# Kernel optimization log

Hardware: AMD Instinct MI355X
Metric: run time of the kernel (lower is better)

## Reference

```python
import jax, jax.numpy as jnp
import numpy as np

SP = 4          # window/split size
HEADS = 8       # num_heads
SHIFTS = (0, 2) # shift_sizes


def _rel_pos_index(sp):
    # Same construction as the torch buffer `relative_position_index`.
    coords = np.stack(np.meshgrid(np.arange(sp), np.arange(sp), indexing='ij'))  # [2,sp,sp]
    coords = coords.reshape(2, -1)                                               # [2, sp*sp]
    rel = coords[:, :, None] - coords[:, None, :]                                # [2, N, N]
    rel = rel.transpose(1, 2, 0).astype(np.int64)                                # [N, N, 2]
    rel[..., 0] += sp - 1
    rel[..., 1] += sp - 1
    rel[..., 0] *= 2 * sp - 1
    return rel.sum(-1)  # [N, N]


def _window_attend(xh, qkv_w, lepe_w, bias, sp, heads, scale):
    # xh: [B, c, H, W] with c = split_dim
    B, c, H, W = xh.shape
    hd = c // heads
    h, w = H // sp, W // sp
    # 1x1 conv to qkv (no bias)
    qkv = jnp.einsum('oi,bihw->bohw', qkv_w, xh)
    q, k, v = jnp.split(qkv, 3, axis=1)
    # depthwise 3x3 LePE on v
    lepe = jax.lax.conv_general_dilated(v, lepe_w, (1, 1), 'SAME',
                                        feature_group_count=c)

    def part(t):
        # 'b (c head) (h hsp) (w wsp) -> (b h w) head (hsp wsp) c'
        t = t.reshape(B, hd, heads, h, sp, w, sp)
        t = t.transpose(0, 3, 5, 2, 4, 6, 1)  # b,h,w,head,hsp,wsp,hd
        return t.reshape(B * h * w, heads, sp * sp, hd)

    q, k, v, lepe = map(part, (q, k, v, lepe))
    attn = jnp.einsum('nhqc,nhkc->nhqk', q * scale, k) + bias[None]  # [N,heads,16,16]
    attn = jax.nn.softmax(attn, axis=-1)
    out = jnp.einsum('nhqk,nhkc->nhqc', attn, v) + lepe
    # inverse rearrange back to [B, c, H, W]
    out = out.reshape(B, h, w, heads, sp, sp, hd)
    out = out.transpose(0, 6, 3, 1, 4, 2, 5).reshape(B, c, H, W)
    return out


def setup_inputs() -> dict:
    key = jax.random.key(0)
    k1, k2, k3, k4 = jax.random.split(key, 4)
    x = jax.random.normal(k1, (8, 128, 192, 192), dtype=jnp.float32)
    qkv_w = jax.random.normal(k2, (192, 64), dtype=jnp.float32) * 0.05   # [3*split_dim, split_dim]
    lepe_w = jax.random.normal(k3, (64, 1, 3, 3), dtype=jnp.float32) * 0.05  # depthwise
    bias_table = jax.random.normal(k4, (49, 8), dtype=jnp.float32) * 0.02    # [(2sp-1)^2, heads]
    return {'x': x, 'qkv_w': qkv_w, 'lepe_w': lepe_w, 'bias_table': bias_table}


def reference(x, qkv_w, lepe_w, bias_table):
    B, C, H, W = x.shape
    c = C // 2
    hd = c // HEADS
    scale = hd ** -0.5
    idx = _rel_pos_index(SP)  # static numpy [16,16]
    bias = bias_table[idx.reshape(-1)].reshape(SP * SP, SP * SP, HEADS)
    bias = bias.transpose(2, 0, 1)  # [heads, 16, 16]

    results = []
    for s in SHIFTS:
        # NOTE: faithful to source, roll is over dims (1,2) = (channel, height)
        xs = jnp.roll(x, (-s, -s), axis=(1, 2)) if s > 0 else x
        halves = (xs[:, :c], xs[:, c:])
        outs = [_window_attend(xh, qkv_w, lepe_w, bias, SP, HEADS, scale)
                for xh in halves]
        if s > 0:
            outs = [jnp.roll(o, (s, s), axis=(1, 2)) for o in outs]
        results.append(jnp.concatenate(outs, axis=1))
    return results[0] + results[1]
```

## Files before the change

### kernel.cpp

```cpp
#include <hip/hip_runtime.h>

typedef __attribute__((ext_vector_type(8))) short short8v;
typedef __attribute__((ext_vector_type(8))) __fp16 h8v;
typedef __attribute__((ext_vector_type(2))) __fp16 h2v;
typedef __attribute__((ext_vector_type(4))) float f32x4;

#define XSTRIDE 136

__device__ inline unsigned short f2bf(float f) {
    unsigned u = __builtin_bit_cast(unsigned, f);
    return (unsigned short)((u + 0x7FFFu + ((u >> 16) & 1u)) >> 16);
}

__device__ inline float dot2(h2v a, h2v b, float c) {
#if __has_builtin(__builtin_amdgcn_fdot2)
    return __builtin_amdgcn_fdot2(a, b, c, false);
#else
    return c + (float)a[0] * (float)b[0] + (float)a[1] * (float)b[1];
#endif
}
__device__ inline h2v pk2h(float a, float b) {
#if __has_builtin(__builtin_amdgcn_cvt_pkrtz)
    return __builtin_bit_cast(h2v, __builtin_amdgcn_cvt_pkrtz(a, b));
#else
    h2v r; r[0] = (__fp16)a; r[1] = (__fp16)b; return r;
#endif
}
__device__ inline float fexp2(float x) {
#if __has_builtin(__builtin_amdgcn_exp2f)
    return __builtin_amdgcn_exp2f(x);
#else
    return __expf(x * 0.6931471805599453f);
#endif
}

__global__ __launch_bounds__(256) void prep_weights(const float* __restrict__ qkv_w,
                                                    __fp16* __restrict__ wf) {
    int it = blockIdx.x * 256 + threadIdx.x;
    if (it >= 1536) return;
    int l = it & 63, frag = it >> 6;
    int which = frag >> 3, nt = (frag >> 1) & 3, kst = frag & 1;
    const float* src = qkv_w + (which * 64 + nt * 16 + (l & 15)) * 64 + kst * 32 + (l >> 4) * 8;
    h8v pk;
    #pragma unroll
    for (int j = 0; j < 8; ++j) pk[j] = (__fp16)src[j];
    *reinterpret_cast<h8v*>(wf + it * 8) = pk;
}

__global__ __launch_bounds__(256) void prep_x(const float* __restrict__ x,
                                              __fp16* __restrict__ xh) {
    const int xt = blockIdx.x;
    const int y  = blockIdx.y;
    const int b  = blockIdx.z;
    const int x0 = xt * 32;
    __shared__ float buf[128 * 33];

    for (int it = threadIdx.x; it < 1024; it += 256) {
        int c = it >> 3, xq = it & 7;
        const float4 v = *reinterpret_cast<const float4*>(
            x + ((b * 128 + c) * 192 + y) * 192 + x0 + xq * 4);
        float* d = &buf[c * 33 + xq * 4];
        d[0] = v.x; d[1] = v.y; d[2] = v.z; d[3] = v.w;
    }
    __syncthreads();

    for (int it = threadIdx.x; it < 512; it += 256) {
        int xl = it >> 4, c8 = it & 15;
        h8v pk;
        #pragma unroll
        for (int j = 0; j < 8; ++j) pk[j] = (__fp16)buf[(c8 * 8 + j) * 33 + xl];
        __fp16* dst = xh + (((size_t)(b * 192 + y) * 192) + x0 + xl) * XSTRIDE + c8 * 8;
        __builtin_memcpy(dst, &pk, 16);
    }
    if (threadIdx.x < 32) {
        int xl = threadIdx.x;
        h2v d2; d2[0] = (__fp16)buf[0 * 33 + xl]; d2[1] = (__fp16)buf[1 * 33 + xl];
        __fp16* dst = xh + (((size_t)(b * 192 + y) * 192) + x0 + xl) * XSTRIDE + 128;
        __builtin_memcpy(dst, &d2, 4);
    }
}

template<int SHIFT, bool ACCUM>
__global__ __launch_bounds__(256) void swin_main(
    const __fp16* __restrict__ xh,
    const __fp16* __restrict__ wfrag,
    const float* __restrict__ lepe_w,
    const float* __restrict__ bias_table,
    float* __restrict__ out)
{
    const int bx = blockIdx.x;
    const int wy = bx / 12, strip = bx % 12;
    const int half = blockIdx.y, b = blockIdx.z;
    const int tid = threadIdx.x;
    const int w = tid >> 6, l = tid & 63;

    __shared__ __fp16 pool[9216];
    __shared__ __fp16 qs[64 * 64];
    __shared__ __fp16 ks[64 * 64];
    __shared__ float  bias_s[392];
    __shared__ __fp16 lepe_s[576];

    for (int i = tid; i < 392; i += 256) bias_s[i] = bias_table[i] * 1.4426950408889634f;
    for (int i = tid; i < 576; i += 256) {
        int d = i & 7, rest = i >> 3;
        int j = rest % 9, h = rest / 9;
        lepe_s[i] = (__fp16)lepe_w[(d * 8 + h) * 9 + j];
    }

    const int ry0 = wy * 4 - 1, rx0 = strip * 16 - 1;
    for (int it = tid; it < 864; it += 256) {
        const int pos = it >> 3, slot = it & 7;
        const int py = pos / 18, px = pos - py * 18;
        const int ry = ry0 + py, rx = rx0 + px;
        h8v val;
        #pragma unroll
        for (int j = 0; j < 8; ++j) val[j] = (__fp16)0.f;
        if (ry >= 0 && ry < 192 && rx >= 0 && rx < 192) {
            int phys = ry + SHIFT; if (phys >= 192) phys -= 192;
            const int srcslot = slot ^ (pos & 7);
            const __fp16* src = xh + (((size_t)(b * 192 + phys) * 192) + rx) * XSTRIDE
                                   + half * 64 + srcslot * 8 + SHIFT;
            __builtin_memcpy(&val, src, 16);
        }
        *reinterpret_cast<h8v*>(&pool[pos * 64 + slot * 8]) = val;
    }
    __syncthreads();

    const int tok16 = l & 15, g = l >> 4;
    h8v Aq[2], Av[3][2];
    {
        const int posq = (1 + (tok16 >> 2)) * 18 + w * 4 + 1 + (tok16 & 3);
        #pragma unroll
        for (int kst = 0; kst < 2; ++kst) {
            int chunk = (kst * 4 + g) ^ (posq & 7);
            Aq[kst] = *reinterpret_cast<const h8v*>(&pool[posq * 64 + chunk * 8]);
        }
        #pragma unroll
        for (int mt = 0; mt < 3; ++mt) {
            int t = mt * 16 + tok16;
            int posv = (t < 36) ? ((t / 6) * 18 + w * 4 + (t % 6)) : 0;
            #pragma unroll
            for (int kst = 0; kst < 2; ++kst) {
                int chunk = (kst * 4 + g) ^ (posv & 7);
                Av[mt][kst] = *reinterpret_cast<const h8v*>(&pool[posv * 64 + chunk * 8]);
            }
        }
    }
    __syncthreads();

    #pragma unroll
    for (int nt = 0; nt < 4; ++nt) {
        h8v Bq[2], Bk[2], Bv[2];
        #pragma unroll
        for (int kst = 0; kst < 2; ++kst) {
            Bq[kst] = *reinterpret_cast<const h8v*>(wfrag + (((0 * 8 + nt * 2 + kst) * 64 + l) * 8));
            Bk[kst] = *reinterpret_cast<const h8v*>(wfrag + (((1 * 8 + nt * 2 + kst) * 64 + l) * 8));
            Bv[kst] = *reinterpret_cast<const h8v*>(wfrag + (((2 * 8 + nt * 2 + kst) * 64 + l) * 8));
        }
        f32x4 aQ = {0.f,0.f,0.f,0.f}, aK = {0.f,0.f,0.f,0.f};
        f32x4 aV[3];
        #pragma unroll
        for (int mt = 0; mt < 3; ++mt) aV[mt] = (f32x4){0.f,0.f,0.f,0.f};
        #pragma unroll
        for (int kst = 0; kst < 2; ++kst) {
            aQ = __builtin_amdgcn_mfma_f32_16x16x32_f16(Aq[kst], Bq[kst], aQ, 0, 0, 0);
            aK = __builtin_amdgcn_mfma_f32_16x16x32_f16(Aq[kst], Bk[kst], aK, 0, 0, 0);
            #pragma unroll
            for (int mt = 0; mt < 3; ++mt)
                aV[mt] = __builtin_amdgcn_mfma_f32_16x16x32_f16(Av[mt][kst], Bv[kst], aV[mt], 0, 0, 0);
        }
        const int ch  = nt * 16 + tok16;
        const int chp = (ch & 7) * 8 + (ch >> 3);
        #pragma unroll
        for (int r = 0; r < 4; ++r) {
            const int qtok = w * 16 + 4 * g + r;
            const int pb = (((chp >> 3) ^ (qtok & 7)) * 8 + (chp & 7));
            qs[qtok * 64 + pb] = (__fp16)(aQ[r] * 0.5101293f);
            ks[qtok * 64 + pb] = (__fp16)aK[r];
        }
        #pragma unroll
        for (int mt = 0; mt < 3; ++mt)
            #pragma unroll
            for (int r = 0; r < 4; ++r) {
                const int t = mt * 16 + 4 * g + r;
                if (t < 36) {
                    const int pb = (((chp >> 3) ^ (t & 7)) * 8 + (chp & 7));
                    pool[(w * 36 + t) * 64 + pb] = (__fp16)aV[mt][r];
                }
            }
    }
    __syncthreads();

    {
        const int h = l >> 3, tqp = l & 7;
        const int qy0 = tqp >> 2, qx0 = tqp & 3;
        const __fp16* vv = &pool[w * 36 * 64];

        const int ox = strip * 16 + w * 4 + qx0;
        int oy0 = wy * 4 + qy0 + SHIFT;     if (oy0 >= 192) oy0 -= 192;
        int oy1 = wy * 4 + qy0 + 2 + SHIFT; if (oy1 >= 192) oy1 -= 192;
        const int ddelta = (oy1 - oy0) * 192;
        int idx0[8];
        float prev0[8], prev1[8];
        #pragma unroll
        for (int d = 0; d < 8; ++d) {
            const int oc = half * 64 + ((d * 8 + h + SHIFT) & 63);
            idx0[d] = ((b * 128 + oc) * 192 + oy0) * 192 + ox;
            if (ACCUM) { prev0[d] = out[idx0[d]]; prev1[d] = out[idx0[d] + ddelta]; }
        }

        const int t0 = w * 16 + tqp, t1 = t0 + 8;
        h8v q0 = *reinterpret_cast<const h8v*>(&qs[t0 * 64 + (h ^ (t0 & 7)) * 8]);
        h8v q1 = *reinterpret_cast<const h8v*>(&qs[t1 * 64 + (h ^ (t1 & 7)) * 8]);
        const h2v* q0p = reinterpret_cast<const h2v*>(&q0);
        const h2v* q1p = reinterpret_cast<const h2v*>(&q1);

        h2v scp0[8], scp1[8];
        float den0 = 0.f, den1 = 0.f;
        #pragma unroll
        for (int tkp = 0; tkp < 8; ++tkp) {
            float e0[2], e1[2];
            #pragma unroll
            for (int u = 0; u < 2; ++u) {
                const int tk = tkp * 2 + u;
                const int kt = w * 16 + tk;
                h8v kr = *reinterpret_cast<const h8v*>(&ks[kt * 64 + (h ^ (kt & 7)) * 8]);
                const h2v* kp = reinterpret_cast<const h2v*>(&kr);
                float s0 = 0.f, s1 = 0.f;
                #pragma unroll
                for (int i = 0; i < 4; ++i) { s0 = dot2(q0p[i], kp[i], s0); s1 = dot2(q1p[i], kp[i], s1); }
                const int ky = tk >> 2, kx = tk & 3;
                s0 += bias_s[((qy0 - ky + 3) * 7 + (qx0 - kx + 3)) * 8 + h];
                s1 += bias_s[((qy0 + 2 - ky + 3) * 7 + (qx0 - kx + 3)) * 8 + h];
                e0[u] = fexp2(s0); e1[u] = fexp2(s1);
            }
            den0 += e0[0] + e0[1]; den1 += e1[0] + e1[1];
            scp0[tkp] = pk2h(e0[0], e0[1]);
            scp1[tkp] = pk2h(e1[0], e1[1]);
        }
        const float inv0 = 1.f / den0, inv1 = 1.f / den1;
        const h2v ip0 = pk2h(inv0, inv0), ip1 = pk2h(inv1, inv1);

        h2v o0pk[4], o1pk[4];
        #pragma unroll
        for (int j = 0; j < 4; ++j) { o0pk[j] = pk2h(0.f, 0.f); o1pk[j] = pk2h(0.f, 0.f); }
        #pragma unroll
        for (int tkp = 0; tkp < 8; ++tkp) {
            const h2v w0 = scp0[tkp] * ip0;
            const h2v w1 = scp1[tkp] * ip1;
            #pragma unroll
            for (int u = 0; u < 2; ++u) {
                const int tk = tkp * 2 + u;
                const int t = (1 + (tk >> 2)) * 6 + 1 + (tk & 3);
                h8v vr = *reinterpret_cast<const h8v*>(&vv[t * 64 + (h ^ (t & 7)) * 8]);
                const h2v* vp = reinterpret_cast<const h2v*>(&vr);
                h2v b0; b0[0] = w0[u]; b0[1] = w0[u];
                h2v b1; b1[0] = w1[u]; b1[1] = w1[u];
                #pragma unroll
                for (int j = 0; j < 4; ++j) {
                    o0pk[j] += b0 * vp[j];
                    o1pk[j] += b1 * vp[j];
                }
            }
        }

        #pragma unroll
        for (int dy = 0; dy < 3; ++dy)
            #pragma unroll
            for (int dx = 0; dx < 3; ++dx) {
                const int ta = (qy0 + dy) * 6 + qx0 + dx;
                const int tb = ta + 12;
                h8v v0 = *reinterpret_cast<const h8v*>(&vv[ta * 64 + (h ^ (ta & 7)) * 8]);
                h8v v1 = *reinterpret_cast<const h8v*>(&vv[tb * 64 + (h ^ (tb & 7)) * 8]);
                h8v lw = *reinterpret_cast<const h8v*>(&lepe_s[(h * 9 + dy * 3 + dx) * 8]);
                const h2v* v0p = reinterpret_cast<const h2v*>(&v0);
                const h2v* v1p = reinterpret_cast<const h2v*>(&v1);
                const h2v* lwp = reinterpret_cast<const h2v*>(&lw);
                #pragma unroll
                for (int j = 0; j < 4; ++j) {
                    o0pk[j] += v0p[j] * lwp[j];
                    o1pk[j] += v1p[j] * lwp[j];
                }
            }

        #pragma unroll
        for (int d = 0; d < 8; ++d) {
            const float a0 = (float)o0pk[d >> 1][d & 1];
            const float a1 = (float)o1pk[d >> 1][d & 1];
            if (ACCUM) { out[idx0[d]] = prev0[d] + a0; out[idx0[d] + ddelta] = prev1[d] + a1; }
            else       { out[idx0[d]] = a0;            out[idx0[d] + ddelta] = a1; }
        }
    }
}

template<int SHIFT, bool ACCUM>
__global__ __launch_bounds__(256) void swin_fb(
    const float* __restrict__ x, const float* __restrict__ qkv_w,
    const float* __restrict__ lepe_w, const float* __restrict__ bias_table,
    float* __restrict__ out)
{
    const int C = 128, HH = 192, WW = 192;
    const int win = blockIdx.x, wy = win / 48, wx = win % 48;
    const int half = blockIdx.y, b = blockIdx.z, tid = threadIdx.x;
    __shared__ short xpA[8 * 64 * 8];
    __shared__ float vs[64 * 37], qsf[64 * 17], ksf[64 * 17];
    __shared__ float bias_s[392], lepe_s[576];
    const int ys0 = wy * 4, xs0 = wx * 4;
    for (int i = tid; i < 392; i += 256) bias_s[i] = bias_table[i];
    for (int i = tid; i < 576; i += 256) lepe_s[i] = lepe_w[i];
    for (int item = tid; item < 512; item += 256) {
        const int slot = item >> 6, l = item & 63, kst = slot & 1;
        int p = 0; bool tvalid = true;
        if (slot < 6) { int t48 = (slot >> 1) * 16 + (l & 15); tvalid = (t48 < 36); p = t48; }
        else { int ti = l & 15; p = (1 + (ti >> 2)) * 6 + 1 + (ti & 3); }
        const int c0 = kst * 32 + (l >> 4) * 8;
        short8v pk;
        #pragma unroll
        for (int j = 0; j < 8; ++j) pk[j] = 0;
        if (tvalid) {
            int py = p / 6, px = p - py * 6;
            int ry = ys0 - 1 + py, rx = xs0 - 1 + px;
            if (ry >= 0 && ry < HH && rx >= 0 && rx < WW) {
                int oy = ry + SHIFT; if (oy >= HH) oy -= HH;
                #pragma unroll
                for (int j = 0; j < 8; ++j) {
                    int oc = half * 64 + c0 + j + SHIFT; if (oc >= C) oc -= C;
                    pk[j] = (short)f2bf(x[((b * C + oc) * HH + oy) * WW + rx]);
                }
            }
        }
        *reinterpret_cast<short8v*>(&xpA[item * 8]) = pk;
    }
    const int w = tid >> 6, l = tid & 63, nn = l & 15, g = l >> 4;
    short8v Bq[2], Bk[2], Bv[2];
    #pragma unroll
    for (int kst = 0; kst < 2; ++kst) {
        const int coff = kst * 32 + g * 8;
        const float* s0 = qkv_w + (w * 16 + nn) * 64 + coff;
        const float* s1 = qkv_w + (64 + w * 16 + nn) * 64 + coff;
        const float* s2 = qkv_w + (128 + w * 16 + nn) * 64 + coff;
        short8v p0, p1, p2;
        #pragma unroll
        for (int j = 0; j < 8; ++j) { p0[j] = (short)f2bf(s0[j]); p1[j] = (short)f2bf(s1[j]); p2[j] = (short)f2bf(s2[j]); }
        Bq[kst] = p0; Bk[kst] = p1; Bv[kst] = p2;
    }
    __syncthreads();
    {
        short8v Aq[2], Avf[3][2];
        #pragma unroll
        for (int kst = 0; kst < 2; ++kst)
            Aq[kst] = *reinterpret_cast<const short8v*>(&xpA[((6 + kst) * 64 + l) * 8]);
        #pragma unroll
        for (int mt = 0; mt < 3; ++mt)
            #pragma unroll
            for (int kst = 0; kst < 2; ++kst)
                Avf[mt][kst] = *reinterpret_cast<const short8v*>(&xpA[((mt * 2 + kst) * 64 + l) * 8]);
        f32x4 aQ = {0,0,0,0}, aK = {0,0,0,0}; f32x4 aV[3];
        #pragma unroll
        for (int mt = 0; mt < 3; ++mt) aV[mt] = (f32x4){0,0,0,0};
        #pragma unroll
        for (int kst = 0; kst < 2; ++kst) {
            aQ = __builtin_amdgcn_mfma_f32_16x16x32_bf16(Aq[kst], Bq[kst], aQ, 0, 0, 0);
            aK = __builtin_amdgcn_mfma_f32_16x16x32_bf16(Aq[kst], Bk[kst], aK, 0, 0, 0);
            #pragma unroll
            for (int mt = 0; mt < 3; ++mt)
                aV[mt] = __builtin_amdgcn_mfma_f32_16x16x32_bf16(Avf[mt][kst], Bv[kst], aV[mt], 0, 0, 0);
        }
        const int ch = w * 16 + nn;
        #pragma unroll
        for (int r = 0; r < 4; ++r) { qsf[ch * 17 + g * 4 + r] = aQ[r]; ksf[ch * 17 + g * 4 + r] = aK[r]; }
        #pragma unroll
        for (int mt = 0; mt < 3; ++mt)
            #pragma unroll
            for (int r = 0; r < 4; ++r) { int tok = mt * 16 + g * 4 + r; if (tok < 36) vs[ch * 37 + tok] = aV[mt][r]; }
    }
    __syncthreads();
    {
        const int tq = tid & 15, h = (tid >> 4) & 7, dh = tid >> 7;
        const int qy = tq >> 2, qx = tq & 3;
        const float scale = 0.35355339059327373f;
        float qreg[8];
        #pragma unroll
        for (int d = 0; d < 8; ++d) qreg[d] = qsf[(d * 8 + h) * 17 + tq] * scale;
        float sc[16]; float m = -1e30f;
        #pragma unroll
        for (int tk = 0; tk < 16; ++tk) {
            float s = 0.f;
            #pragma unroll
            for (int d = 0; d < 8; ++d) s += qreg[d] * ksf[(d * 8 + h) * 17 + tk];
            s += bias_s[((qy - (tk >> 2) + 3) * 7 + (qx - (tk & 3) + 3)) * 8 + h];
            sc[tk] = s; m = fmaxf(m, s);
        }
        float den = 0.f;
        #pragma unroll
        for (int tk = 0; tk < 16; ++tk) { sc[tk] = __expf(sc[tk] - m); den += sc[tk]; }
        const float inv = 1.f / den;
        float lw[4][9];
        #pragma unroll
        for (int dd = 0; dd < 4; ++dd) {
            int ch = (dh * 4 + dd) * 8 + h;
            #pragma unroll
            for (int j = 0; j < 9; ++j) lw[dd][j] = lepe_s[ch * 9 + j];
        }
        float o[4] = {0,0,0,0};
        #pragma unroll
        for (int tk = 0; tk < 16; ++tk) {
            int p = (1 + (tk >> 2)) * 6 + 1 + (tk & 3); float s = sc[tk];
            #pragma unroll
            for (int dd = 0; dd < 4; ++dd) o[dd] += s * vs[((dh * 4 + dd) * 8 + h) * 37 + p];
        }
        int oy = ys0 + qy + SHIFT; if (oy >= HH) oy -= HH;
        const int irx = xs0 + qx;
        #pragma unroll
        for (int dd = 0; dd < 4; ++dd) {
            const int ch = (dh * 4 + dd) * 8 + h;
            float val = o[dd] * inv;
            #pragma unroll
            for (int dy = 0; dy < 3; ++dy)
                #pragma unroll
                for (int dx = 0; dx < 3; ++dx)
                    val += vs[ch * 37 + (qy + dy) * 6 + (qx + dx)] * lw[dd][dy * 3 + dx];
            const int oc = half * 64 + ((ch + SHIFT) & 63);
            const int oidx = ((b * C + oc) * HH + oy) * WW + irx;
            if (ACCUM) out[oidx] += val; else out[oidx] = val;
        }
    }
}

extern "C" void kernel_launch(void* const* d_in, const int* in_sizes, int n_in,
                              void* d_out, int out_size, void* d_ws, size_t ws_size,
                              hipStream_t stream) {
    const float* x          = (const float*)d_in[0];
    const float* qkv_w      = (const float*)d_in[1];
    const float* lepe_w     = (const float*)d_in[2];
    const float* bias_table = (const float*)d_in[3];
    float* out = (float*)d_out;

    const size_t XH_BYTES = 8UL * 192 * 192 * XSTRIDE * 2;
    const size_t NEED = 32768 + XH_BYTES;

    if (ws_size >= NEED) {
        __fp16* wf = (__fp16*)d_ws;
        __fp16* xh = (__fp16*)((char*)d_ws + 32768);
        prep_weights<<<6, 256, 0, stream>>>(qkv_w, wf);
        prep_x<<<dim3(6, 192, 8), 256, 0, stream>>>(x, xh);
        dim3 grid(576, 2, 8);
        swin_main<0, false><<<grid, 256, 0, stream>>>(xh, wf, lepe_w, bias_table, out);
        swin_main<2, true ><<<grid, 256, 0, stream>>>(xh, wf, lepe_w, bias_table, out);
    } else {
        dim3 grid(48 * 48, 2, 8);
        swin_fb<0, false><<<grid, 256, 0, stream>>>(x, qkv_w, lepe_w, bias_table, out);
        swin_fb<2, true ><<<grid, 256, 0, stream>>>(x, qkv_w, lepe_w, bias_table, out);
    }
}
```

Measured before the change: 325.4 us.

## Pre-roll fp16 input per shift and pass Q through lane shuffles instead of LDS

prep_x now writes two fully rolled, unpadded fp16 copies of x (shift 0 and shift 2), so the main kernel loads aligned 16-byte vectors with no row wrap or channel offset. Q is no longer staged in shared memory. It is packed to half2 and redistributed with cross-lane shuffles into each lane's registers for the attention step. This removes the unaligned XSTRIDE-136 loads and the Q LDS buffer, but doubles the prep write traffic and workspace and adds shuffle and select work.

```diff
diff --git a/kernel.cpp b/kernel.cpp
--- a/kernel.cpp
+++ b/kernel.cpp
@@ -4,8 +4,6 @@
 typedef __attribute__((ext_vector_type(8))) __fp16 h8v;
 typedef __attribute__((ext_vector_type(2))) __fp16 h2v;
 typedef __attribute__((ext_vector_type(4))) float f32x4;
-
-#define XSTRIDE 136
 
 __device__ inline unsigned short f2bf(float f) {
     unsigned u = __builtin_bit_cast(unsigned, f);
@@ -32,6 +30,13 @@
 #else
     return __expf(x * 0.6931471805599453f);
 #endif
+}
+__device__ inline h2v sel_pack(int x01, int x23, int y01, int y23, int rSel) {
+    unsigned sx = (unsigned)(rSel < 2 ? x01 : x23);
+    unsigned sy = (unsigned)(rSel < 2 ? y01 : y23);
+    unsigned ex = (rSel & 1) ? (sx >> 16) : (sx & 0xffffu);
+    unsigned ey = (rSel & 1) ? (sy >> 16) : (sy & 0xffffu);
+    return __builtin_bit_cast(h2v, (unsigned)(ex | (ey << 16)));
 }
 
 __global__ __launch_bounds__(256) void prep_weights(const float* __restrict__ qkv_w,
@@ -48,7 +53,8 @@
 }
 
 __global__ __launch_bounds__(256) void prep_x(const float* __restrict__ x,
-                                              __fp16* __restrict__ xh) {
+                                              __fp16* __restrict__ xbf0,
+                                              __fp16* __restrict__ xbf2) {
     const int xt = blockIdx.x;
     const int y  = blockIdx.y;
     const int b  = blockIdx.z;
@@ -64,25 +70,27 @@
     }
     __syncthreads();
 
-    for (int it = threadIdx.x; it < 512; it += 256) {
-        int xl = it >> 4, c8 = it & 15;
-        h8v pk;
-        #pragma unroll
-        for (int j = 0; j < 8; ++j) pk[j] = (__fp16)buf[(c8 * 8 + j) * 33 + xl];
-        __fp16* dst = xh + (((size_t)(b * 192 + y) * 192) + x0 + xl) * XSTRIDE + c8 * 8;
-        __builtin_memcpy(dst, &pk, 16);
-    }
-    if (threadIdx.x < 32) {
-        int xl = threadIdx.x;
-        h2v d2; d2[0] = (__fp16)buf[0 * 33 + xl]; d2[1] = (__fp16)buf[1 * 33 + xl];
-        __fp16* dst = xh + (((size_t)(b * 192 + y) * 192) + x0 + xl) * XSTRIDE + 128;
-        __builtin_memcpy(dst, &d2, 4);
+    #pragma unroll
+    for (int si = 0; si < 2; ++si) {
+        const int s = si * 2;
+        __fp16* dst = si ? xbf2 : xbf0;
+        int ydst = y - s; if (ydst < 0) ydst += 192;
+        for (int it = threadIdx.x; it < 512; it += 256) {
+            int xl = it >> 4, c8 = it & 15;
+            h8v pk;
+            #pragma unroll
+            for (int j = 0; j < 8; ++j) {
+                int c = (s + c8 * 8 + j) & 127;
+                pk[j] = (__fp16)buf[c * 33 + xl];
+            }
+            *reinterpret_cast<h8v*>(dst + (((size_t)(b * 192 + ydst) * 192) + x0 + xl) * 128 + c8 * 8) = pk;
+        }
     }
 }
 
 template<int SHIFT, bool ACCUM>
 __global__ __launch_bounds__(256) void swin_main(
-    const __fp16* __restrict__ xh,
+    const __fp16* __restrict__ xbf,
     const __fp16* __restrict__ wfrag,
     const float* __restrict__ lepe_w,
     const float* __restrict__ bias_table,
@@ -95,7 +103,6 @@
     const int w = tid >> 6, l = tid & 63;
 
     __shared__ __fp16 pool[9216];
-    __shared__ __fp16 qs[64 * 64];
     __shared__ __fp16 ks[64 * 64];
     __shared__ float  bias_s[392];
     __shared__ __fp16 lepe_s[576];
@@ -116,11 +123,9 @@
         #pragma unroll
         for (int j = 0; j < 8; ++j) val[j] = (__fp16)0.f;
         if (ry >= 0 && ry < 192 && rx >= 0 && rx < 192) {
-            int phys = ry + SHIFT; if (phys >= 192) phys -= 192;
             const int srcslot = slot ^ (pos & 7);
-            const __fp16* src = xh + (((size_t)(b * 192 + phys) * 192) + rx) * XSTRIDE
-                                   + half * 64 + srcslot * 8 + SHIFT;
-            __builtin_memcpy(&val, src, 16);
+            val = *reinterpret_cast<const h8v*>(
+                xbf + (((size_t)(b * 192 + ry) * 192) + rx) * 128 + half * 64 + srcslot * 8);
         }
         *reinterpret_cast<h8v*>(&pool[pos * 64 + slot * 8]) = val;
     }
@@ -148,6 +153,11 @@
     }
     __syncthreads();
 
+    const int h = l >> 3, tqp = l & 7;
+    const int pA = ((tqp >> 2) << 4) + h;
+    const int rSel = tqp & 3;
+    h2v q0p[4], q1p[4];
+
     #pragma unroll
     for (int nt = 0; nt < 4; ++nt) {
         h8v Bq[2], Bk[2], Bv[2];
@@ -169,14 +179,26 @@
             for (int mt = 0; mt < 3; ++mt)
                 aV[mt] = __builtin_amdgcn_mfma_f32_16x16x32_f16(Av[mt][kst], Bv[kst], aV[mt], 0, 0, 0);
         }
+
+        {
+            const float QS = 0.5101293f;
+            int pk01 = (int)__builtin_bit_cast(unsigned, pk2h(aQ[0] * QS, aQ[1] * QS));
+            int pk23 = (int)__builtin_bit_cast(unsigned, pk2h(aQ[2] * QS, aQ[3] * QS));
+            int a01 = __shfl(pk01, pA),      a23 = __shfl(pk23, pA);
+            int b01 = __shfl(pk01, pA + 8),  b23 = __shfl(pk23, pA + 8);
+            int c01 = __shfl(pk01, pA + 32), c23 = __shfl(pk23, pA + 32);
+            int d01 = __shfl(pk01, pA + 40), d23 = __shfl(pk23, pA + 40);
+            q0p[nt] = sel_pack(a01, a23, b01, b23, rSel);
+            q1p[nt] = sel_pack(c01, c23, d01, d23, rSel);
+        }
+
         const int ch  = nt * 16 + tok16;
         const int chp = (ch & 7) * 8 + (ch >> 3);
         #pragma unroll
         for (int r = 0; r < 4; ++r) {
-            const int qtok = w * 16 + 4 * g + r;
-            const int pb = (((chp >> 3) ^ (qtok & 7)) * 8 + (chp & 7));
-            qs[qtok * 64 + pb] = (__fp16)(aQ[r] * 0.5101293f);
-            ks[qtok * 64 + pb] = (__fp16)aK[r];
+            const int ktok = w * 16 + 4 * g + r;
+            const int pb = (((chp >> 3) ^ (ktok & 7)) * 8 + (chp & 7));
+            ks[ktok * 64 + pb] = (__fp16)aK[r];
         }
         #pragma unroll
         for (int mt = 0; mt < 3; ++mt)
@@ -192,7 +214,6 @@
     __syncthreads();
 
     {
-        const int h = l >> 3, tqp = l & 7;
         const int qy0 = tqp >> 2, qx0 = tqp & 3;
         const __fp16* vv = &pool[w * 36 * 64];
 
@@ -208,12 +229,6 @@
             idx0[d] = ((b * 128 + oc) * 192 + oy0) * 192 + ox;
             if (ACCUM) { prev0[d] = out[idx0[d]]; prev1[d] = out[idx0[d] + ddelta]; }
         }
-
-        const int t0 = w * 16 + tqp, t1 = t0 + 8;
-        h8v q0 = *reinterpret_cast<const h8v*>(&qs[t0 * 64 + (h ^ (t0 & 7)) * 8]);
-        h8v q1 = *reinterpret_cast<const h8v*>(&qs[t1 * 64 + (h ^ (t1 & 7)) * 8]);
-        const h2v* q0p = reinterpret_cast<const h2v*>(&q0);
-        const h2v* q1p = reinterpret_cast<const h2v*>(&q1);
 
         h2v scp0[8], scp1[8];
         float den0 = 0.f, den1 = 0.f;
@@ -436,17 +451,18 @@
     const float* bias_table = (const float*)d_in[3];
     float* out = (float*)d_out;
 
-    const size_t XH_BYTES = 8UL * 192 * 192 * XSTRIDE * 2;
-    const size_t NEED = 32768 + XH_BYTES;
+    const size_t XBF_BYTES = 8UL * 192 * 192 * 128 * 2;
+    const size_t NEED = 32768 + 2 * XBF_BYTES;
 
     if (ws_size >= NEED) {
-        __fp16* wf = (__fp16*)d_ws;
-        __fp16* xh = (__fp16*)((char*)d_ws + 32768);
+        __fp16* wf   = (__fp16*)d_ws;
+        __fp16* xbf0 = (__fp16*)((char*)d_ws + 32768);
+        __fp16* xbf2 = (__fp16*)((char*)d_ws + 32768 + XBF_BYTES);
         prep_weights<<<6, 256, 0, stream>>>(qkv_w, wf);
-        prep_x<<<dim3(6, 192, 8), 256, 0, stream>>>(x, xh);
+        prep_x<<<dim3(6, 192, 8), 256, 0, stream>>>(x, xbf0, xbf2);
         dim3 grid(576, 2, 8);
-        swin_main<0, false><<<grid, 256, 0, stream>>>(xh, wf, lepe_w, bias_table, out);
-        swin_main<2, true ><<<grid, 256, 0, stream>>>(xh, wf, lepe_w, bias_table, out);
+        swin_main<0, false><<<grid, 256, 0, stream>>>(xbf0, wf, lepe_w, bias_table, out);
+        swin_main<2, true ><<<grid, 256, 0, stream>>>(xbf2, wf, lepe_w, bias_table, out);
     } else {
         dim3 grid(48 * 48, 2, 8);
         swin_fb<0, false><<<grid, 256, 0, stream>>>(x, qkv_w, lepe_w, bias_table, out);
```

New measurement: 402.8 us. 1.24x slower.
